# Kernel optimization log

Hardware: AMD Instinct MI355X
Metric: run time of the kernel (lower is better)

## Reference

```python
import jax, jax.numpy as jnp
import numpy as np

MAX_LEVEL = 4
CURV = 1.0
MAX_NORM = 0.95
N_ITER = 10


def project_to_poincare(x):
    # Rescale points whose norm exceeds max_norm / sqrt(c) back onto the ball.
    norm = jnp.linalg.norm(x, axis=-1, keepdims=True)
    max_r = MAX_NORM / jnp.sqrt(jnp.asarray(CURV, x.dtype))
    return jnp.where(norm > max_r, x / (norm + 1e-12) * max_r, x)


def poincare_distance(x, y):
    # d(x,y) = arccosh(1 + 2c||x-y||^2 / ((1-c||x||^2)(1-c||y||^2))) / sqrt(c)
    sq = jnp.sum((x - y) ** 2, axis=-1)
    nx = jnp.sum(x * x, axis=-1)
    ny = jnp.sum(y * y, axis=-1)
    denom = jnp.maximum((1.0 - CURV * nx) * (1.0 - CURV * ny), 1e-12)
    arg = 1.0 + 2.0 * CURV * sq / denom
    return jnp.arccosh(jnp.maximum(arg, 1.0 + 1e-7)) / jnp.sqrt(CURV)


def setup_inputs() -> dict:
    key = jax.random.key(0)
    k1, k2 = jax.random.split(key)
    B, D = 1048576, 32
    z = jax.random.normal(k1, (B, D), dtype=jnp.float32)
    batch_indices = jax.random.randint(k2, (B,), 0, 19683, dtype=jnp.int64)
    level_weights = jnp.array([0.5 ** i for i in range(MAX_LEVEL)], dtype=jnp.float32)
    return {"z": z, "batch_indices": batch_indices, "level_weights": level_weights}


def reference(z, batch_indices, level_weights):
    z_hyp = project_to_poincare(z)
    B = z.shape[0]
    ones = jnp.ones((B,), dtype=z.dtype)
    total_loss = jnp.asarray(0.0, dtype=z.dtype)
    for level in range(1, MAX_LEVEL + 1):
        n_seg = 3 ** level
        seg = (batch_indices // (3 ** (9 - level))).astype(jnp.int32)
        counts = jax.ops.segment_sum(ones, seg, num_segments=n_seg)          # [n_seg]
        sums = jax.ops.segment_sum(z_hyp, seg, num_segments=n_seg)           # [n_seg, D]
        safe_counts = jnp.maximum(counts, 1.0)[:, None]
        euc_mean = sums / safe_counts                                        # weighted (uniform) mean
        # Frechet-mean iteration: direction = sum_i w_i (x_i - mean) = euc_mean - mean
        mean = project_to_poincare(euc_mean)
        for _ in range(N_ITER):
            mean = project_to_poincare(mean + 0.1 * (euc_mean - mean))
        cent = mean[seg]                                                     # [B, D]
        dists = poincare_distance(z_hyp, cent)                               # [B]
        dist_mean = jax.ops.segment_sum(dists, seg, num_segments=n_seg) / jnp.maximum(counts, 1.0)
        valid = counts >= 2.0                                                # clusters with <2 pts skipped
        level_loss = jnp.sum(jnp.where(valid, dist_mean, 0.0))
        n_unique = jnp.sum(counts > 0.0)
        total_loss = total_loss + level_weights[level - 1] * level_loss / jnp.maximum(n_unique, 1.0)
    return total_loss
```

## Files before the change

kernel.cpp:

```cpp
#include <hip/hip_runtime.h>
#include <math.h>


#define MAXR  0.95f
#define MAXR2 0.9025f
#define LN2F  0.6931471805599453f

#define NPART 1024
#define HCOLS 2673
#define OFF_HSUM8 (NPART * HCOLS)
#define OFF_DSUM  (OFF_HSUM8 + 8 * HCOLS)
#define OFF_CENT  (OFF_DSUM + 8 * 324)
#define OFF_CNT   (OFF_CENT + 120 * 32)
#define OFF_CN4   (OFF_CNT + 120)
#define OFF_TI4   (OFF_CN4 + 324)

__device__ __forceinline__ float fsqrt(float x) { return __builtin_amdgcn_sqrtf(x); }
__device__ __forceinline__ float frcp(float x)  { return __builtin_amdgcn_rcpf(x); }
__device__ __forceinline__ float frsq(float x)  { return __builtin_amdgcn_rsqf(x); }

__device__ __forceinline__ float red8_dpp(float v) {
    v += __int_as_float(__builtin_amdgcn_update_dpp(0, __float_as_int(v), 0xB1, 0xF, 0xF, 1));
    v += __int_as_float(__builtin_amdgcn_update_dpp(0, __float_as_int(v), 0x4E, 0xF, 0xF, 1));
    v += __int_as_float(__builtin_amdgcn_update_dpp(0, __float_as_int(v), 0x141, 0xF, 0xF, 1));
    return v;
}

__device__ __forceinline__ float red32_dpp(float v) {
    v += __int_as_float(__builtin_amdgcn_update_dpp(0, __float_as_int(v), 0xB1, 0xF, 0xF, 1));
    v += __int_as_float(__builtin_amdgcn_update_dpp(0, __float_as_int(v), 0x4E, 0xF, 0xF, 1));
    v += __int_as_float(__builtin_amdgcn_update_dpp(0, __float_as_int(v), 0x141, 0xF, 0xF, 1));
    v += __int_as_float(__builtin_amdgcn_update_dpp(0, __float_as_int(v), 0x140, 0xF, 0xF, 1));
    v += __shfl_xor(v, 16, 32);
    return v;
}

__device__ __forceinline__ int dup_rank(int s4, int g, int sub) {
    int sj = __shfl(s4, sub * 8, 64);
    unsigned long long eq = __ballot(sj == s4);
    unsigned int row = (unsigned int)(eq >> (g * 8));
    return __popc(row & ((1u << g) - 1u));
}

__global__ __launch_bounds__(256) void pass1_hist(
        const float* __restrict__ z, const int* __restrict__ idx,
        float* __restrict__ part, int B) {
    __shared__ float lsum[4][81][36];
    const int tid = threadIdx.x;
    for (int j = tid; j < 4 * 81 * 36; j += 256) (&lsum[0][0][0])[j] = 0.f;
    __syncthreads();

    const int w = tid >> 6;
    const int g = (tid & 63) >> 3;
    const int sub = tid & 7;
    const int STRIDE = gridDim.x * 128;
    const int base0 = blockIdx.x * 128 + w * 32 + g;
    const int nfull = B / STRIDE;
    float* const lw = &lsum[w][0][0];

    for (int it = 0; it < nfull; ++it) {
        const int ib = it * STRIDE + base0;
        float4 xv[4];
        int s4v[4], rank[4];
#pragma unroll
        for (int b = 0; b < 4; ++b)
            xv[b] = *(const float4*)(z + (size_t)(ib + b * 8) * 32 + sub * 4);
#pragma unroll
        for (int b = 0; b < 4; ++b)
            s4v[b] = idx[ib + b * 8] / 243;
#pragma unroll
        for (int b = 0; b < 4; ++b) {
            const float nx = red8_dpp(xv[b].x * xv[b].x + xv[b].y * xv[b].y +
                                      xv[b].z * xv[b].z + xv[b].w * xv[b].w);
            const float s = (nx > MAXR2) ? MAXR * frsq(nx) : 1.0f;
            xv[b].x *= s; xv[b].y *= s; xv[b].z *= s; xv[b].w *= s;
        }
#pragma unroll
        for (int b = 0; b < 4; ++b)
            rank[b] = dup_rank(s4v[b], g, sub);
#pragma unroll
        for (int b = 0; b < 4; ++b) {
            float* row = lw + s4v[b] * 36;
            for (int r = 0;; ++r) {
                if (!__any(rank[b] == r)) break;
                if (rank[b] == r) {
                    float4 cur = *(float4*)(row + sub * 4);
                    cur.x += xv[b].x; cur.y += xv[b].y;
                    cur.z += xv[b].z; cur.w += xv[b].w;
                    *(float4*)(row + sub * 4) = cur;
                    if (sub == 0) row[32] += 1.0f;
                }
            }
        }
    }
    if (B % STRIDE) {
        const int ib = nfull * STRIDE + base0;
        for (int b = 0; b < 4; ++b) {
            const int i = ib + b * 8;
            const bool act = i < B;
            float4 xv = act ? *(const float4*)(z + (size_t)i * 32 + sub * 4)
                            : make_float4(0.f, 0.f, 0.f, 0.f);
            int s4 = act ? idx[i] / 243 : 81 + g;
            const float nx = red8_dpp(xv.x * xv.x + xv.y * xv.y +
                                      xv.z * xv.z + xv.w * xv.w);
            const float s = (nx > MAXR2) ? MAXR * frsq(nx) : 1.0f;
            xv.x *= s; xv.y *= s; xv.z *= s; xv.w *= s;
            int rank = dup_rank(s4, g, sub);
            for (int r = 0;; ++r) {
                if (!__any(rank == r)) break;
                if (act && rank == r) {
                    float* row = lw + s4 * 36;
                    float4 cur = *(float4*)(row + sub * 4);
                    cur.x += xv.x; cur.y += xv.y; cur.z += xv.z; cur.w += xv.w;
                    *(float4*)(row + sub * 4) = cur;
                    if (sub == 0) row[32] += 1.0f;
                }
            }
        }
    }
    __syncthreads();
    float* myslice = part + (size_t)blockIdx.x * HCOLS;
    for (int j = tid; j < HCOLS; j += 256) {
        const int r = j / 33, c = j - r * 33;
        myslice[j] = lsum[0][r][c] + lsum[1][r][c] +
                     lsum[2][r][c] + lsum[3][r][c];
    }
}

__global__ __launch_bounds__(256) void pass2a_reduce(
        const float* __restrict__ part, float* __restrict__ hsum8,
        float* __restrict__ dsum) {
    const int tid = threadIdx.x;
    const int group = blockIdx.x / 11;
    const int jb = blockIdx.x - group * 11;
    const int j = jb * 256 + tid;
    if (blockIdx.x == 0)
        for (int k = tid; k < 8 * 324; k += 256) dsum[k] = 0.f;
    if (j < HCOLS) {
        const float* p0 = part + (size_t)(group * 128) * HCOLS + j;
        float s0 = 0.f, s1 = 0.f, s2 = 0.f, s3 = 0.f;
        for (int b = 0; b < 128; b += 4) {
            s0 += p0[(size_t)b * HCOLS];
            s1 += p0[(size_t)(b + 1) * HCOLS];
            s2 += p0[(size_t)(b + 2) * HCOLS];
            s3 += p0[(size_t)(b + 3) * HCOLS];
        }
        hsum8[group * HCOLS + j] = (s0 + s1) + (s2 + s3);
    }
}

__global__ __launch_bounds__(256) void pass2_centroids(
        const float* __restrict__ hsum8,
        float* __restrict__ cent, float* __restrict__ cnt_all,
        float* __restrict__ cnorm4, int* __restrict__ tidx4) {
    __shared__ float euc[120][33];
    __shared__ float cn[120];
    const int tid = threadIdx.x;
    for (int j = tid; j < HCOLS; j += 256) {
        float s = 0.f;
#pragma unroll
        for (int p = 0; p < 8; ++p) s += hsum8[p * HCOLS + j];
        const int r = j / 33, c = j - r * 33;
        euc[39 + r][c] = s;
    }
    __syncthreads();
    for (int j = tid; j < 27 * 33; j += 256) {
        const int r = j / 33, c = j - r * 33;
        euc[12 + r][c] = euc[39 + 3 * r][c] + euc[40 + 3 * r][c] + euc[41 + 3 * r][c];
    }
    __syncthreads();
    for (int j = tid; j < 9 * 33; j += 256) {
        const int r = j / 33, c = j - r * 33;
        euc[3 + r][c] = euc[12 + 3 * r][c] + euc[13 + 3 * r][c] + euc[14 + 3 * r][c];
    }
    __syncthreads();
    for (int j = tid; j < 3 * 33; j += 256) {
        const int r = j / 33, c = j - r * 33;
        euc[r][c] = euc[3 + 3 * r][c] + euc[4 + 3 * r][c] + euc[5 + 3 * r][c];
    }
    __syncthreads();
    const int lane = tid & 31;
    const int grp = tid >> 5;
    for (int t = grp; t < 120; t += 8) {
        const float sum = euc[t][lane];
        const float cnt = euc[t][32];
        const float em = sum / fmaxf(cnt, 1.0f);
        float m = em;
        {
            float norm = sqrtf(red32_dpp(m * m));
            if (norm > MAXR) m *= MAXR / (norm + 1e-12f);
        }
        for (int it = 0; it < 10; ++it) {
            float v = m + 0.1f * (em - m);
            float norm = sqrtf(red32_dpp(v * v));
            if (norm > MAXR) v *= MAXR / (norm + 1e-12f);
            m = v;
        }
        cent[t * 32 + lane] = m;
        float ny = red32_dpp(m * m);
        if (lane == 0) { cnt_all[t] = cnt; cn[t] = 1.0f - ny; }
    }
    __syncthreads();
    if (tid < 81) {
        const int s4 = tid;
        const int d3 = s4 / 3, d9 = d3 / 3, d27 = d9 / 3;
        const int t0 = d27, t1 = 3 + d9, t2 = 12 + d3, t3 = 39 + s4;
        ((int4*)tidx4)[s4] = make_int4(t0, t1, t2, t3);
        ((float4*)cnorm4)[s4] = make_float4(cn[t0], cn[t1], cn[t2], cn[t3]);
    }
}

__global__ __launch_bounds__(256) void pass3_dist(
        const float* __restrict__ z, const int* __restrict__ idx,
        const float* __restrict__ cent, const float* __restrict__ cnorm4,
        const int* __restrict__ tidx4, float* __restrict__ dsum, int B) {
    __shared__ float lcent[120 * 32];
    __shared__ float4 lcn4[81];
    __shared__ int4 ltl4[81];
    __shared__ float ld[4][81][4];
    const int tid = threadIdx.x;
    for (int j = tid; j < 120 * 32; j += 256) lcent[j] = cent[j];
    for (int j = tid; j < 324; j += 256) ((float*)lcn4)[j] = cnorm4[j];
    for (int j = tid; j < 324; j += 256) ((int*)ltl4)[j] = tidx4[j];
    for (int j = tid; j < 4 * 81 * 4; j += 256) (&ld[0][0][0])[j] = 0.f;
    __syncthreads();

    const int w = tid >> 6;
    const int g = (tid & 63) >> 3;
    const int sub = tid & 7;
    const int STRIDE = gridDim.x * 128;
    const int base0 = blockIdx.x * 128 + w * 32 + g;
    const int nfull = B / STRIDE;

    for (int it = 0; it < nfull; ++it) {
        const int ib = it * STRIDE + base0;
        float4 xv[4];
        int s4v[4], rank[4];
        float dl[4][4];
#pragma unroll
        for (int b = 0; b < 4; ++b)
            xv[b] = *(const float4*)(z + (size_t)(ib + b * 8) * 32 + sub * 4);
#pragma unroll
        for (int b = 0; b < 4; ++b)
            s4v[b] = idx[ib + b * 8] / 243;
#pragma unroll
        for (int b = 0; b < 4; ++b) {
            float nx = red8_dpp(xv[b].x * xv[b].x + xv[b].y * xv[b].y +
                                xv[b].z * xv[b].z + xv[b].w * xv[b].w);
            const float s = (nx > MAXR2) ? MAXR * frsq(nx) : 1.0f;
            xv[b].x *= s; xv[b].y *= s; xv[b].z *= s; xv[b].w *= s;
            nx = nx * s * s;
            const float ah = 0.5f * (1.0f - nx);
            const float c2a = 1.0f + nx;
            const int s4 = s4v[b];
            const int4 t4 = ltl4[s4];
            const float4 cn4 = lcn4[s4];
            const int tls[4] = {t4.x, t4.y, t4.z, t4.w};
            const float bnys[4] = {cn4.x, cn4.y, cn4.z, cn4.w};
#pragma unroll
            for (int l = 0; l < 4; ++l) {
                const int t = tls[l];
                const float4 c = *(const float4*)(lcent + t * 32 + sub * 4);
                const float dot = red8_dpp(xv[b].x * c.x + xv[b].y * c.y +
                                           xv[b].z * c.z + xv[b].w * c.w);
                const float bny = bnys[l];
                const float sq = fmaf(-2.0f, dot, c2a - bny);
                const float d = fmaxf(ah * bny, 5e-13f);
                float tt = sq * frcp(d);
                tt = fmaxf(tt, 1e-7f);
                dl[b][l] = __log2f(1.0f + tt + fsqrt(tt * (tt + 2.0f)));
            }
        }
#pragma unroll
        for (int b = 0; b < 4; ++b)
            rank[b] = dup_rank(s4v[b], g, sub);
#pragma unroll
        for (int b = 0; b < 4; ++b) {
            float* row = &ld[w][s4v[b]][0];
            for (int r = 0;; ++r) {
                if (!__any(rank[b] == r)) break;
                if (rank[b] == r && sub == 0) {
                    float4 cur = *(float4*)row;
                    cur.x += dl[b][0]; cur.y += dl[b][1];
                    cur.z += dl[b][2]; cur.w += dl[b][3];
                    *(float4*)row = cur;
                }
            }
        }
    }
    if (B % STRIDE) {
        const int ib = nfull * STRIDE + base0;
        for (int b = 0; b < 4; ++b) {
            const int i = ib + b * 8;
            const bool act = i < B;
            float4 xv = act ? *(const float4*)(z + (size_t)i * 32 + sub * 4)
                            : make_float4(0.f, 0.f, 0.f, 0.f);
            int s4 = act ? idx[i] / 243 : 81 + g;
            float nx = red8_dpp(xv.x * xv.x + xv.y * xv.y + xv.z * xv.z + xv.w * xv.w);
            const float s = (nx > MAXR2) ? MAXR * frsq(nx) : 1.0f;
            xv.x *= s; xv.y *= s; xv.z *= s; xv.w *= s;
            nx = nx * s * s;
            const float ah = 0.5f * (1.0f - nx);
            const float c2a = 1.0f + nx;
            const int ss = act ? s4 : 0;
            const int4 t4 = ltl4[ss];
            const float4 cn4 = lcn4[ss];
            const int tls[4] = {t4.x, t4.y, t4.z, t4.w};
            const float bnys[4] = {cn4.x, cn4.y, cn4.z, cn4.w};
            float dl[4];
#pragma unroll
            for (int l = 0; l < 4; ++l) {
                const int t = tls[l];
                const float4 c = *(const float4*)(lcent + t * 32 + sub * 4);
                const float dot = red8_dpp(xv.x * c.x + xv.y * c.y +
                                           xv.z * c.z + xv.w * c.w);
                const float bny = bnys[l];
                const float sq = fmaf(-2.0f, dot, c2a - bny);
                const float d = fmaxf(ah * bny, 5e-13f);
                float tt = sq * frcp(d);
                tt = fmaxf(tt, 1e-7f);
                dl[l] = __log2f(1.0f + tt + fsqrt(tt * (tt + 2.0f)));
            }
            int rank = dup_rank(s4, g, sub);
            for (int r = 0;; ++r) {
                if (!__any(rank == r)) break;
                if (act && rank == r && sub == 0) {
                    float* row = &ld[w][s4][0];
                    float4 cur = *(float4*)row;
                    cur.x += dl[0]; cur.y += dl[1]; cur.z += dl[2]; cur.w += dl[3];
                    *(float4*)row = cur;
                }
            }
        }
    }
    __syncthreads();
    float* dpart = dsum + (blockIdx.x & 7) * 324;
    for (int j = tid; j < 81 * 4; j += 256) {
        const float v = (&ld[0][0][0])[j] + (&ld[1][0][0])[j] +
                        (&ld[2][0][0])[j] + (&ld[3][0][0])[j];
        unsafeAtomicAdd(&dpart[j], v);
    }
}

__global__ __launch_bounds__(128) void pass4_final(
        const float* __restrict__ dsum, const float* __restrict__ cnt_all,
        const float* __restrict__ w, float* __restrict__ out) {
    __shared__ float sl[81];
    __shared__ float su[81];
    const int tid = threadIdx.x;
    const int toff[4] = {0, 3, 12, 39};
    const int nsegs[4] = {3, 9, 27, 81};
    float total = 0.f;
    for (int l = 0; l < 4; ++l) {
        const int n_seg = nsegs[l];
        const int ch = 81 / n_seg;
        __syncthreads();
        if (tid < n_seg) {
            float cnt = cnt_all[toff[l] + tid];
            float ds = 0.f;
            for (int p = 0; p < 8; ++p)
                for (int k = 0; k < ch; ++k)
                    ds += dsum[p * 324 + (tid * ch + k) * 4 + l];
            sl[tid] = (cnt >= 2.0f) ? ds * LN2F / fmaxf(cnt, 1.0f) : 0.f;
            su[tid] = (cnt > 0.0f) ? 1.f : 0.f;
        }
        __syncthreads();
        if (tid == 0) {
            float ll = 0.f, nu = 0.f;
            for (int s = 0; s < n_seg; ++s) { ll += sl[s]; nu += su[s]; }
            total += w[l] * ll / fmaxf(nu, 1.0f);
        }
    }
    if (tid == 0) out[0] = total;
}

extern "C" void kernel_launch(void* const* d_in, const int* in_sizes, int n_in,
                              void* d_out, int out_size, void* d_ws, size_t ws_size,
                              hipStream_t stream) {
    const float* z   = (const float*)d_in[0];
    const int*   idx = (const int*)d_in[1];
    const float* w   = (const float*)d_in[2];
    float* out = (float*)d_out;
    float* ws  = (float*)d_ws;
    const int B = in_sizes[1];

    float* part    = ws;
    float* hsum8   = ws + OFF_HSUM8;
    float* dsum    = ws + OFF_DSUM;
    float* cent    = ws + OFF_CENT;
    float* cnt_all = ws + OFF_CNT;
    float* cnorm4  = ws + OFF_CN4;
    int*   tidx4   = (int*)(ws + OFF_TI4);

    pass1_hist<<<NPART, 256, 0, stream>>>(z, idx, part, B);
    pass2a_reduce<<<88, 256, 0, stream>>>(part, hsum8, dsum);
    pass2_centroids<<<1, 256, 0, stream>>>(hsum8, cent, cnt_all, cnorm4, tidx4);
    pass3_dist<<<2048, 256, 0, stream>>>(z, idx, cent, cnorm4, tidx4, dsum, B);
    pass4_final<<<1, 128, 0, stream>>>(dsum, cnt_all, w, out);
}
```

Measured before the change: 122.7 us.

## Prefetch next iteration loads and spread distance transcendentals across sub-lanes

Both streaming kernels now software-pipeline their global loads, fetching the next iteration's z rows and indices while the current batch is processed, to hide memory latency. In the distance pass, each of the eight sub-lanes still computes all four dot products, but only lanes 0-3 evaluate the arccosh for their own level. This replaces four redundant per-lane transcendental chains with one, and the shared-memory accumulation becomes a scalar add per level lane. The distance grid size also drops from 2048 to 1792 blocks. The cost is higher register pressure from the prefetch buffers, which may lower occupancy.

```diff
diff --git a/kernel.cpp b/kernel.cpp
--- a/kernel.cpp
+++ b/kernel.cpp
@@ -58,16 +58,28 @@
     const int nfull = B / STRIDE;
     float* const lw = &lsum[w][0][0];
 
+    float4 xv[4];
+    int s4v[4];
+    if (nfull > 0) {
+#pragma unroll
+        for (int b = 0; b < 4; ++b) {
+            xv[b] = *(const float4*)(z + (size_t)(base0 + b * 8) * 32 + sub * 4);
+            s4v[b] = idx[base0 + b * 8] / 243;
+        }
+    }
     for (int it = 0; it < nfull; ++it) {
-        const int ib = it * STRIDE + base0;
-        float4 xv[4];
-        int s4v[4], rank[4];
-#pragma unroll
-        for (int b = 0; b < 4; ++b)
-            xv[b] = *(const float4*)(z + (size_t)(ib + b * 8) * 32 + sub * 4);
-#pragma unroll
-        for (int b = 0; b < 4; ++b)
-            s4v[b] = idx[ib + b * 8] / 243;
+        float4 xn[4];
+        int sn[4];
+        const bool more = (it + 1) < nfull;
+        if (more) {
+            const int ibn = (it + 1) * STRIDE + base0;
+#pragma unroll
+            for (int b = 0; b < 4; ++b) {
+                xn[b] = *(const float4*)(z + (size_t)(ibn + b * 8) * 32 + sub * 4);
+                sn[b] = idx[ibn + b * 8] / 243;
+            }
+        }
+        int rank[4];
 #pragma unroll
         for (int b = 0; b < 4; ++b) {
             const float nx = red8_dpp(xv[b].x * xv[b].x + xv[b].y * xv[b].y +
@@ -92,26 +104,29 @@
                 }
             }
         }
+        if (more) {
+#pragma unroll
+            for (int b = 0; b < 4; ++b) { xv[b] = xn[b]; s4v[b] = sn[b]; }
+        }
     }
     if (B % STRIDE) {
         const int ib = nfull * STRIDE + base0;
         for (int b = 0; b < 4; ++b) {
             const int i = ib + b * 8;
             const bool act = i < B;
-            float4 xv = act ? *(const float4*)(z + (size_t)i * 32 + sub * 4)
-                            : make_float4(0.f, 0.f, 0.f, 0.f);
+            float4 x = act ? *(const float4*)(z + (size_t)i * 32 + sub * 4)
+                           : make_float4(0.f, 0.f, 0.f, 0.f);
             int s4 = act ? idx[i] / 243 : 81 + g;
-            const float nx = red8_dpp(xv.x * xv.x + xv.y * xv.y +
-                                      xv.z * xv.z + xv.w * xv.w);
+            const float nx = red8_dpp(x.x * x.x + x.y * x.y + x.z * x.z + x.w * x.w);
             const float s = (nx > MAXR2) ? MAXR * frsq(nx) : 1.0f;
-            xv.x *= s; xv.y *= s; xv.z *= s; xv.w *= s;
+            x.x *= s; x.y *= s; x.z *= s; x.w *= s;
             int rank = dup_rank(s4, g, sub);
             for (int r = 0;; ++r) {
                 if (!__any(rank == r)) break;
                 if (act && rank == r) {
                     float* row = lw + s4 * 36;
                     float4 cur = *(float4*)(row + sub * 4);
-                    cur.x += xv.x; cur.y += xv.y; cur.z += xv.z; cur.w += xv.w;
+                    cur.x += x.x; cur.y += x.y; cur.z += x.z; cur.w += x.w;
                     *(float4*)(row + sub * 4) = cur;
                     if (sub == 0) row[32] += 1.0f;
                 }
@@ -215,12 +230,12 @@
         const float* __restrict__ cent, const float* __restrict__ cnorm4,
         const int* __restrict__ tidx4, float* __restrict__ dsum, int B) {
     __shared__ float lcent[120 * 32];
-    __shared__ float4 lcn4[81];
+    __shared__ float lcn[81 * 4];
     __shared__ int4 ltl4[81];
     __shared__ float ld[4][81][4];
     const int tid = threadIdx.x;
     for (int j = tid; j < 120 * 32; j += 256) lcent[j] = cent[j];
-    for (int j = tid; j < 324; j += 256) ((float*)lcn4)[j] = cnorm4[j];
+    for (int j = tid; j < 324; j += 256) lcn[j] = cnorm4[j];
     for (int j = tid; j < 324; j += 256) ((int*)ltl4)[j] = tidx4[j];
     for (int j = tid; j < 4 * 81 * 4; j += 256) (&ld[0][0][0])[j] = 0.f;
     __syncthreads();
@@ -228,21 +243,36 @@
     const int w = tid >> 6;
     const int g = (tid & 63) >> 3;
     const int sub = tid & 7;
+    const int lvl = sub & 3;
+    const bool sb1 = (sub & 1) != 0;
+    const bool sb2 = (sub & 2) != 0;
     const int STRIDE = gridDim.x * 128;
     const int base0 = blockIdx.x * 128 + w * 32 + g;
     const int nfull = B / STRIDE;
 
+    float4 xv[4];
+    int s4v[4];
+    if (nfull > 0) {
+#pragma unroll
+        for (int b = 0; b < 4; ++b) {
+            xv[b] = *(const float4*)(z + (size_t)(base0 + b * 8) * 32 + sub * 4);
+            s4v[b] = idx[base0 + b * 8] / 243;
+        }
+    }
     for (int it = 0; it < nfull; ++it) {
-        const int ib = it * STRIDE + base0;
-        float4 xv[4];
-        int s4v[4], rank[4];
-        float dl[4][4];
-#pragma unroll
-        for (int b = 0; b < 4; ++b)
-            xv[b] = *(const float4*)(z + (size_t)(ib + b * 8) * 32 + sub * 4);
-#pragma unroll
-        for (int b = 0; b < 4; ++b)
-            s4v[b] = idx[ib + b * 8] / 243;
+        float4 xn[4];
+        int sn[4];
+        const bool more = (it + 1) < nfull;
+        if (more) {
+            const int ibn = (it + 1) * STRIDE + base0;
+#pragma unroll
+            for (int b = 0; b < 4; ++b) {
+                xn[b] = *(const float4*)(z + (size_t)(ibn + b * 8) * 32 + sub * 4);
+                sn[b] = idx[ibn + b * 8] / 243;
+            }
+        }
+        int rank[4];
+        float dlv[4];
 #pragma unroll
         for (int b = 0; b < 4; ++b) {
             float nx = red8_dpp(xv[b].x * xv[b].x + xv[b].y * xv[b].y +
@@ -254,38 +284,44 @@
             const float c2a = 1.0f + nx;
             const int s4 = s4v[b];
             const int4 t4 = ltl4[s4];
-            const float4 cn4 = lcn4[s4];
-            const int tls[4] = {t4.x, t4.y, t4.z, t4.w};
-            const float bnys[4] = {cn4.x, cn4.y, cn4.z, cn4.w};
-#pragma unroll
-            for (int l = 0; l < 4; ++l) {
-                const int t = tls[l];
-                const float4 c = *(const float4*)(lcent + t * 32 + sub * 4);
-                const float dot = red8_dpp(xv[b].x * c.x + xv[b].y * c.y +
-                                           xv[b].z * c.z + xv[b].w * c.w);
-                const float bny = bnys[l];
-                const float sq = fmaf(-2.0f, dot, c2a - bny);
-                const float d = fmaxf(ah * bny, 5e-13f);
-                float tt = sq * frcp(d);
-                tt = fmaxf(tt, 1e-7f);
-                dl[b][l] = __log2f(1.0f + tt + fsqrt(tt * (tt + 2.0f)));
-            }
+            const float4 c0 = *(const float4*)(lcent + t4.x * 32 + sub * 4);
+            const float4 c1 = *(const float4*)(lcent + t4.y * 32 + sub * 4);
+            const float4 c2 = *(const float4*)(lcent + t4.z * 32 + sub * 4);
+            const float4 c3 = *(const float4*)(lcent + t4.w * 32 + sub * 4);
+            const float d0 = red8_dpp(xv[b].x * c0.x + xv[b].y * c0.y +
+                                      xv[b].z * c0.z + xv[b].w * c0.w);
+            const float d1 = red8_dpp(xv[b].x * c1.x + xv[b].y * c1.y +
+                                      xv[b].z * c1.z + xv[b].w * c1.w);
+            const float d2 = red8_dpp(xv[b].x * c2.x + xv[b].y * c2.y +
+                                      xv[b].z * c2.z + xv[b].w * c2.w);
+            const float d3 = red8_dpp(xv[b].x * c3.x + xv[b].y * c3.y +
+                                      xv[b].z * c3.z + xv[b].w * c3.w);
+            const float bny = lcn[(s4 << 2) | lvl];
+            const float ta = sb1 ? d1 : d0;
+            const float tb = sb1 ? d3 : d2;
+            const float dsel = sb2 ? tb : ta;
+            const float sq = fmaf(-2.0f, dsel, c2a - bny);
+            const float dd = fmaxf(ah * bny, 5e-13f);
+            float tt = sq * frcp(dd);
+            tt = fmaxf(tt, 1e-7f);
+            dlv[b] = __log2f(1.0f + tt + fsqrt(tt * (tt + 2.0f)));
         }
 #pragma unroll
         for (int b = 0; b < 4; ++b)
             rank[b] = dup_rank(s4v[b], g, sub);
 #pragma unroll
         for (int b = 0; b < 4; ++b) {
-            float* row = &ld[w][s4v[b]][0];
+            float* p = &ld[w][s4v[b]][lvl];
             for (int r = 0;; ++r) {
                 if (!__any(rank[b] == r)) break;
-                if (rank[b] == r && sub == 0) {
-                    float4 cur = *(float4*)row;
-                    cur.x += dl[b][0]; cur.y += dl[b][1];
-                    cur.z += dl[b][2]; cur.w += dl[b][3];
-                    *(float4*)row = cur;
+                if (rank[b] == r && sub < 4) {
+                    *p += dlv[b];
                 }
             }
+        }
+        if (more) {
+#pragma unroll
+            for (int b = 0; b < 4; ++b) { xv[b] = xn[b]; s4v[b] = sn[b]; }
         }
     }
     if (B % STRIDE) {
@@ -293,42 +329,38 @@
         for (int b = 0; b < 4; ++b) {
             const int i = ib + b * 8;
             const bool act = i < B;
-            float4 xv = act ? *(const float4*)(z + (size_t)i * 32 + sub * 4)
-                            : make_float4(0.f, 0.f, 0.f, 0.f);
-            int s4 = act ? idx[i] / 243 : 81 + g;
-            float nx = red8_dpp(xv.x * xv.x + xv.y * xv.y + xv.z * xv.z + xv.w * xv.w);
+            float4 x = act ? *(const float4*)(z + (size_t)i * 32 + sub * 4)
+                           : make_float4(0.f, 0.f, 0.f, 0.f);
+            const int s4 = act ? idx[i] / 243 : 0;
+            float nx = red8_dpp(x.x * x.x + x.y * x.y + x.z * x.z + x.w * x.w);
             const float s = (nx > MAXR2) ? MAXR * frsq(nx) : 1.0f;
-            xv.x *= s; xv.y *= s; xv.z *= s; xv.w *= s;
+            x.x *= s; x.y *= s; x.z *= s; x.w *= s;
             nx = nx * s * s;
             const float ah = 0.5f * (1.0f - nx);
             const float c2a = 1.0f + nx;
-            const int ss = act ? s4 : 0;
-            const int4 t4 = ltl4[ss];
-            const float4 cn4 = lcn4[ss];
-            const int tls[4] = {t4.x, t4.y, t4.z, t4.w};
-            const float bnys[4] = {cn4.x, cn4.y, cn4.z, cn4.w};
-            float dl[4];
-#pragma unroll
-            for (int l = 0; l < 4; ++l) {
-                const int t = tls[l];
-                const float4 c = *(const float4*)(lcent + t * 32 + sub * 4);
-                const float dot = red8_dpp(xv.x * c.x + xv.y * c.y +
-                                           xv.z * c.z + xv.w * c.w);
-                const float bny = bnys[l];
-                const float sq = fmaf(-2.0f, dot, c2a - bny);
-                const float d = fmaxf(ah * bny, 5e-13f);
-                float tt = sq * frcp(d);
-                tt = fmaxf(tt, 1e-7f);
-                dl[l] = __log2f(1.0f + tt + fsqrt(tt * (tt + 2.0f)));
-            }
-            int rank = dup_rank(s4, g, sub);
+            const int4 t4 = ltl4[s4];
+            const float4 c0 = *(const float4*)(lcent + t4.x * 32 + sub * 4);
+            const float4 c1 = *(const float4*)(lcent + t4.y * 32 + sub * 4);
+            const float4 c2 = *(const float4*)(lcent + t4.z * 32 + sub * 4);
+            const float4 c3 = *(const float4*)(lcent + t4.w * 32 + sub * 4);
+            const float d0 = red8_dpp(x.x * c0.x + x.y * c0.y + x.z * c0.z + x.w * c0.w);
+            const float d1 = red8_dpp(x.x * c1.x + x.y * c1.y + x.z * c1.z + x.w * c1.w);
+            const float d2 = red8_dpp(x.x * c2.x + x.y * c2.y + x.z * c2.z + x.w * c2.w);
+            const float d3 = red8_dpp(x.x * c3.x + x.y * c3.y + x.z * c3.z + x.w * c3.w);
+            const float bny = lcn[(s4 << 2) | lvl];
+            const float ta = sb1 ? d1 : d0;
+            const float tb = sb1 ? d3 : d2;
+            const float dsel = sb2 ? tb : ta;
+            const float sq = fmaf(-2.0f, dsel, c2a - bny);
+            const float dd = fmaxf(ah * bny, 5e-13f);
+            float tt = sq * frcp(dd);
+            tt = fmaxf(tt, 1e-7f);
+            const float dl = __log2f(1.0f + tt + fsqrt(tt * (tt + 2.0f)));
+            int rank = dup_rank(act ? s4 : -1 - g, g, sub);
             for (int r = 0;; ++r) {
                 if (!__any(rank == r)) break;
-                if (act && rank == r && sub == 0) {
-                    float* row = &ld[w][s4][0];
-                    float4 cur = *(float4*)row;
-                    cur.x += dl[0]; cur.y += dl[1]; cur.z += dl[2]; cur.w += dl[3];
-                    *(float4*)row = cur;
+                if (act && rank == r && sub < 4) {
+                    ld[w][s4][lvl] += dl;
                 }
             }
         }
@@ -395,6 +427,6 @@
     pass1_hist<<<NPART, 256, 0, stream>>>(z, idx, part, B);
     pass2a_reduce<<<88, 256, 0, stream>>>(part, hsum8, dsum);
     pass2_centroids<<<1, 256, 0, stream>>>(hsum8, cent, cnt_all, cnorm4, tidx4);
-    pass3_dist<<<2048, 256, 0, stream>>>(z, idx, cent, cnorm4, tidx4, dsum, B);
+    pass3_dist<<<1792, 256, 0, stream>>>(z, idx, cent, cnorm4, tidx4, dsum, B);
     pass4_final<<<1, 128, 0, stream>>>(dsum, cnt_all, w, out);
 }
```

Result: slower. 127.0 us (+3.5%).

## Fold single-block centroid and final-reduction kernels into last-block-done tails

Applied to the files above, without the earlier changes.

Removes the separate single-block pass2_centroids and pass4_final launches. Their work now runs in whichever block of the preceding kernel finishes last, detected with an atomic counter and threadfence. This saves two kernel launches and their inter-kernel gaps. It also packs the per-segment tree indices into uchar4 in shared memory and reads partial sums with 64-bit atomic loads. In exchange, it adds counter resets, fences and a serial tail on the last block.

```diff
diff --git a/kernel.cpp b/kernel.cpp
--- a/kernel.cpp
+++ b/kernel.cpp
@@ -8,16 +8,23 @@
 
 #define NPART 1024
 #define HCOLS 2673
+#define HS8   2674
 #define OFF_HSUM8 (NPART * HCOLS)
-#define OFF_DSUM  (OFF_HSUM8 + 8 * HCOLS)
+#define OFF_DSUM  (OFF_HSUM8 + 8 * HS8)
 #define OFF_CENT  (OFF_DSUM + 8 * 324)
 #define OFF_CNT   (OFF_CENT + 120 * 32)
 #define OFF_CN4   (OFF_CNT + 120)
 #define OFF_TI4   (OFF_CN4 + 324)
+#define OFF_CTR   (OFF_TI4 + 324)
 
 __device__ __forceinline__ float fsqrt(float x) { return __builtin_amdgcn_sqrtf(x); }
 __device__ __forceinline__ float frcp(float x)  { return __builtin_amdgcn_rcpf(x); }
 __device__ __forceinline__ float frsq(float x)  { return __builtin_amdgcn_rsqf(x); }
+
+__device__ __forceinline__ unsigned long long aload64(const float* p) {
+    return __hip_atomic_load((const unsigned long long*)p,
+                             __ATOMIC_RELAXED, __HIP_MEMORY_SCOPE_AGENT);
+}
 
 __device__ __forceinline__ float red8_dpp(float v) {
     v += __int_as_float(__builtin_amdgcn_update_dpp(0, __float_as_int(v), 0xB1, 0xF, 0xF, 1));
@@ -44,9 +51,10 @@
 
 __global__ __launch_bounds__(256) void pass1_hist(
         const float* __restrict__ z, const int* __restrict__ idx,
-        float* __restrict__ part, int B) {
+        float* __restrict__ part, unsigned int* __restrict__ ctr, int B) {
     __shared__ float lsum[4][81][36];
     const int tid = threadIdx.x;
+    if (blockIdx.x == 0 && tid == 0) { ctr[0] = 0u; ctr[1] = 0u; }
     for (int j = tid; j < 4 * 81 * 36; j += 256) (&lsum[0][0][0])[j] = 0.f;
     __syncthreads();
 
@@ -98,20 +106,19 @@
         for (int b = 0; b < 4; ++b) {
             const int i = ib + b * 8;
             const bool act = i < B;
-            float4 xv = act ? *(const float4*)(z + (size_t)i * 32 + sub * 4)
-                            : make_float4(0.f, 0.f, 0.f, 0.f);
+            float4 x = act ? *(const float4*)(z + (size_t)i * 32 + sub * 4)
+                           : make_float4(0.f, 0.f, 0.f, 0.f);
             int s4 = act ? idx[i] / 243 : 81 + g;
-            const float nx = red8_dpp(xv.x * xv.x + xv.y * xv.y +
-                                      xv.z * xv.z + xv.w * xv.w);
+            const float nx = red8_dpp(x.x * x.x + x.y * x.y + x.z * x.z + x.w * x.w);
             const float s = (nx > MAXR2) ? MAXR * frsq(nx) : 1.0f;
-            xv.x *= s; xv.y *= s; xv.z *= s; xv.w *= s;
+            x.x *= s; x.y *= s; x.z *= s; x.w *= s;
             int rank = dup_rank(s4, g, sub);
             for (int r = 0;; ++r) {
                 if (!__any(rank == r)) break;
                 if (act && rank == r) {
                     float* row = lw + s4 * 36;
                     float4 cur = *(float4*)(row + sub * 4);
-                    cur.x += xv.x; cur.y += xv.y; cur.z += xv.z; cur.w += xv.w;
+                    cur.x += x.x; cur.y += x.y; cur.z += x.z; cur.w += x.w;
                     *(float4*)(row + sub * 4) = cur;
                     if (sub == 0) row[32] += 1.0f;
                 }
@@ -127,9 +134,14 @@
     }
 }
 
-__global__ __launch_bounds__(256) void pass2a_reduce(
+__global__ __launch_bounds__(256) void pass2ab(
         const float* __restrict__ part, float* __restrict__ hsum8,
-        float* __restrict__ dsum) {
+        float* __restrict__ dsum, float* __restrict__ cent,
+        float* __restrict__ cnt_all, float* __restrict__ cnorm4,
+        int* __restrict__ tidx4, unsigned int* __restrict__ ctr) {
+    __shared__ float euc[120][33];
+    __shared__ float cn[120];
+    __shared__ int amLast;
     const int tid = threadIdx.x;
     const int group = blockIdx.x / 11;
     const int jb = blockIdx.x - group * 11;
@@ -145,37 +157,43 @@
             s2 += p0[(size_t)(b + 2) * HCOLS];
             s3 += p0[(size_t)(b + 3) * HCOLS];
         }
-        hsum8[group * HCOLS + j] = (s0 + s1) + (s2 + s3);
-    }
-}
-
-__global__ __launch_bounds__(256) void pass2_centroids(
-        const float* __restrict__ hsum8,
-        float* __restrict__ cent, float* __restrict__ cnt_all,
-        float* __restrict__ cnorm4, int* __restrict__ tidx4) {
-    __shared__ float euc[120][33];
-    __shared__ float cn[120];
-    const int tid = threadIdx.x;
-    for (int j = tid; j < HCOLS; j += 256) {
-        float s = 0.f;
-#pragma unroll
-        for (int p = 0; p < 8; ++p) s += hsum8[p * HCOLS + j];
-        const int r = j / 33, c = j - r * 33;
-        euc[39 + r][c] = s;
-    }
-    __syncthreads();
-    for (int j = tid; j < 27 * 33; j += 256) {
-        const int r = j / 33, c = j - r * 33;
+        hsum8[group * HS8 + j] = (s0 + s1) + (s2 + s3);
+    }
+    __syncthreads();
+    if (tid == 0) {
+        __threadfence();
+        amLast = (atomicAdd(ctr, 1u) == (unsigned)gridDim.x - 1u);
+    }
+    __syncthreads();
+    if (!amLast) return;
+    __threadfence();
+    for (int k = tid; k < 120 * 33; k += 256) (&euc[0][0])[k] = 0.f;
+    __syncthreads();
+    for (int k = tid; k < HS8 / 2; k += 256) {
+        const int j2 = 2 * k;
+        float a = 0.f, b = 0.f;
+#pragma unroll
+        for (int p = 0; p < 8; ++p) {
+            const unsigned long long v = aload64(hsum8 + p * HS8 + j2);
+            a += __uint_as_float((unsigned)v);
+            b += __uint_as_float((unsigned)(v >> 32));
+        }
+        if (j2 < HCOLS)     euc[39 + j2 / 33][j2 % 33] = a;
+        if (j2 + 1 < HCOLS) euc[39 + (j2 + 1) / 33][(j2 + 1) % 33] = b;
+    }
+    __syncthreads();
+    for (int k = tid; k < 27 * 33; k += 256) {
+        const int r = k / 33, c = k - r * 33;
         euc[12 + r][c] = euc[39 + 3 * r][c] + euc[40 + 3 * r][c] + euc[41 + 3 * r][c];
     }
     __syncthreads();
-    for (int j = tid; j < 9 * 33; j += 256) {
-        const int r = j / 33, c = j - r * 33;
+    for (int k = tid; k < 9 * 33; k += 256) {
+        const int r = k / 33, c = k - r * 33;
         euc[3 + r][c] = euc[12 + 3 * r][c] + euc[13 + 3 * r][c] + euc[14 + 3 * r][c];
     }
     __syncthreads();
-    for (int j = tid; j < 3 * 33; j += 256) {
-        const int r = j / 33, c = j - r * 33;
+    for (int k = tid; k < 3 * 33; k += 256) {
+        const int r = k / 33, c = k - r * 33;
         euc[r][c] = euc[3 + 3 * r][c] + euc[4 + 3 * r][c] + euc[5 + 3 * r][c];
     }
     __syncthreads();
@@ -213,15 +231,22 @@
 __global__ __launch_bounds__(256) void pass3_dist(
         const float* __restrict__ z, const int* __restrict__ idx,
         const float* __restrict__ cent, const float* __restrict__ cnorm4,
-        const int* __restrict__ tidx4, float* __restrict__ dsum, int B) {
+        const int* __restrict__ tidx4, float* __restrict__ dsum,
+        const float* __restrict__ cnt_all, const float* __restrict__ wl,
+        float* __restrict__ out, unsigned int* __restrict__ ctr, int B) {
     __shared__ float lcent[120 * 32];
     __shared__ float4 lcn4[81];
-    __shared__ int4 ltl4[81];
+    __shared__ uchar4 ltl4[81];
     __shared__ float ld[4][81][4];
+    __shared__ int amLast;
     const int tid = threadIdx.x;
     for (int j = tid; j < 120 * 32; j += 256) lcent[j] = cent[j];
-    for (int j = tid; j < 324; j += 256) ((float*)lcn4)[j] = cnorm4[j];
-    for (int j = tid; j < 324; j += 256) ((int*)ltl4)[j] = tidx4[j];
+    for (int j = tid; j < 81; j += 256) {
+        lcn4[j] = ((const float4*)cnorm4)[j];
+        const int4 t4 = ((const int4*)tidx4)[j];
+        ltl4[j] = make_uchar4((unsigned char)t4.x, (unsigned char)t4.y,
+                              (unsigned char)t4.z, (unsigned char)t4.w);
+    }
     for (int j = tid; j < 4 * 81 * 4; j += 256) (&ld[0][0][0])[j] = 0.f;
     __syncthreads();
 
@@ -253,7 +278,7 @@
             const float ah = 0.5f * (1.0f - nx);
             const float c2a = 1.0f + nx;
             const int s4 = s4v[b];
-            const int4 t4 = ltl4[s4];
+            const uchar4 t4 = ltl4[s4];
             const float4 cn4 = lcn4[s4];
             const int tls[4] = {t4.x, t4.y, t4.z, t4.w};
             const float bnys[4] = {cn4.x, cn4.y, cn4.z, cn4.w};
@@ -293,18 +318,17 @@
         for (int b = 0; b < 4; ++b) {
             const int i = ib + b * 8;
             const bool act = i < B;
-            float4 xv = act ? *(const float4*)(z + (size_t)i * 32 + sub * 4)
-                            : make_float4(0.f, 0.f, 0.f, 0.f);
-            int s4 = act ? idx[i] / 243 : 81 + g;
-            float nx = red8_dpp(xv.x * xv.x + xv.y * xv.y + xv.z * xv.z + xv.w * xv.w);
+            float4 x = act ? *(const float4*)(z + (size_t)i * 32 + sub * 4)
+                           : make_float4(0.f, 0.f, 0.f, 0.f);
+            const int s4 = act ? idx[i] / 243 : 0;
+            float nx = red8_dpp(x.x * x.x + x.y * x.y + x.z * x.z + x.w * x.w);
             const float s = (nx > MAXR2) ? MAXR * frsq(nx) : 1.0f;
-            xv.x *= s; xv.y *= s; xv.z *= s; xv.w *= s;
+            x.x *= s; x.y *= s; x.z *= s; x.w *= s;
             nx = nx * s * s;
             const float ah = 0.5f * (1.0f - nx);
             const float c2a = 1.0f + nx;
-            const int ss = act ? s4 : 0;
-            const int4 t4 = ltl4[ss];
-            const float4 cn4 = lcn4[ss];
+            const uchar4 t4 = ltl4[s4];
+            const float4 cn4 = lcn4[s4];
             const int tls[4] = {t4.x, t4.y, t4.z, t4.w};
             const float bnys[4] = {cn4.x, cn4.y, cn4.z, cn4.w};
             float dl[4];
@@ -312,8 +336,8 @@
             for (int l = 0; l < 4; ++l) {
                 const int t = tls[l];
                 const float4 c = *(const float4*)(lcent + t * 32 + sub * 4);
-                const float dot = red8_dpp(xv.x * c.x + xv.y * c.y +
-                                           xv.z * c.z + xv.w * c.w);
+                const float dot = red8_dpp(x.x * c.x + x.y * c.y +
+                                           x.z * c.z + x.w * c.w);
                 const float bny = bnys[l];
                 const float sq = fmaf(-2.0f, dot, c2a - bny);
                 const float d = fmaxf(ah * bny, 5e-13f);
@@ -321,7 +345,7 @@
                 tt = fmaxf(tt, 1e-7f);
                 dl[l] = __log2f(1.0f + tt + fsqrt(tt * (tt + 2.0f)));
             }
-            int rank = dup_rank(s4, g, sub);
+            int rank = dup_rank(act ? s4 : -1 - g, g, sub);
             for (int r = 0;; ++r) {
                 if (!__any(rank == r)) break;
                 if (act && rank == r && sub == 0) {
@@ -340,14 +364,29 @@
                         (&ld[2][0][0])[j] + (&ld[3][0][0])[j];
         unsafeAtomicAdd(&dpart[j], v);
     }
-}
-
-__global__ __launch_bounds__(128) void pass4_final(
-        const float* __restrict__ dsum, const float* __restrict__ cnt_all,
-        const float* __restrict__ w, float* __restrict__ out) {
-    __shared__ float sl[81];
-    __shared__ float su[81];
-    const int tid = threadIdx.x;
+    __syncthreads();
+    if (tid == 0) {
+        __threadfence();
+        amLast = (atomicAdd(ctr + 1, 1u) == (unsigned)gridDim.x - 1u);
+    }
+    __syncthreads();
+    if (!amLast) return;
+    __threadfence();
+    float* sdsum = lcent;
+    float* sl = lcent + 324;
+    float* su = lcent + 405;
+    for (int k = tid; k < 162; k += 256) {
+        float a = 0.f, b = 0.f;
+#pragma unroll
+        for (int p = 0; p < 8; ++p) {
+            const unsigned long long v = aload64(dsum + p * 324 + 2 * k);
+            a += __uint_as_float((unsigned)v);
+            b += __uint_as_float((unsigned)(v >> 32));
+        }
+        sdsum[2 * k] = a;
+        sdsum[2 * k + 1] = b;
+    }
+    __syncthreads();
     const int toff[4] = {0, 3, 12, 39};
     const int nsegs[4] = {3, 9, 27, 81};
     float total = 0.f;
@@ -358,9 +397,8 @@
         if (tid < n_seg) {
             float cnt = cnt_all[toff[l] + tid];
             float ds = 0.f;
-            for (int p = 0; p < 8; ++p)
-                for (int k = 0; k < ch; ++k)
-                    ds += dsum[p * 324 + (tid * ch + k) * 4 + l];
+            for (int k = 0; k < ch; ++k)
+                ds += sdsum[(tid * ch + k) * 4 + l];
             sl[tid] = (cnt >= 2.0f) ? ds * LN2F / fmaxf(cnt, 1.0f) : 0.f;
             su[tid] = (cnt > 0.0f) ? 1.f : 0.f;
         }
@@ -368,7 +406,7 @@
         if (tid == 0) {
             float ll = 0.f, nu = 0.f;
             for (int s = 0; s < n_seg; ++s) { ll += sl[s]; nu += su[s]; }
-            total += w[l] * ll / fmaxf(nu, 1.0f);
+            total += wl[l] * ll / fmaxf(nu, 1.0f);
         }
     }
     if (tid == 0) out[0] = total;
@@ -391,10 +429,11 @@
     float* cnt_all = ws + OFF_CNT;
     float* cnorm4  = ws + OFF_CN4;
     int*   tidx4   = (int*)(ws + OFF_TI4);
-
-    pass1_hist<<<NPART, 256, 0, stream>>>(z, idx, part, B);
-    pass2a_reduce<<<88, 256, 0, stream>>>(part, hsum8, dsum);
-    pass2_centroids<<<1, 256, 0, stream>>>(hsum8, cent, cnt_all, cnorm4, tidx4);
-    pass3_dist<<<2048, 256, 0, stream>>>(z, idx, cent, cnorm4, tidx4, dsum, B);
-    pass4_final<<<1, 128, 0, stream>>>(dsum, cnt_all, w, out);
-}
+    unsigned int* ctr = (unsigned int*)(ws + OFF_CTR);
+
+    pass1_hist<<<NPART, 256, 0, stream>>>(z, idx, part, ctr, B);
+    pass2ab<<<88, 256, 0, stream>>>(part, hsum8, dsum, cent, cnt_all,
+                                    cnorm4, tidx4, ctr);
+    pass3_dist<<<2048, 256, 0, stream>>>(z, idx, cent, cnorm4, tidx4, dsum,
+                                         cnt_all, w, out, ctr, B);
+}
```

Result: slower. 178.1 us (+45.1%).
